# Kernel tuning notes

Hardware: AMD Instinct MI355X
Metric: run time of the kernel (lower is better)

Reference implementation:

```python
import jax, jax.numpy as jnp
import numpy as np

B, T, U = 64, 400, 64
V, E, H = 80, 128, 400
M, K = 10, 20  # attention mixtures, output mixtures


def _lstm_cell(x, h, c, W_ih, W_hh, b_ih, b_hh):
    g = x @ W_ih.T + b_ih + h @ W_hh.T + b_hh
    i, f, gg, o = jnp.split(g, 4, axis=-1)
    c_new = jax.nn.sigmoid(f) * c + jax.nn.sigmoid(i) * jnp.tanh(gg)
    h_new = jax.nn.sigmoid(o) * jnp.tanh(c_new)
    return h_new, c_new


def setup_inputs() -> dict:
    key = jax.random.key(0)
    ks = jax.random.split(key, 16)
    s = 0.05
    inp = {
        'strokes': jax.random.normal(ks[0], (B, T, 3), jnp.float32),
        'chars': jax.random.randint(ks[1], (B, U), 0, V, jnp.int32),
        'chars_mask': jnp.ones((B, U), jnp.float32),
        'emb': jax.random.normal(ks[2], (V, E)) * s,
        # layer_0: input 3+E
        'W_ih0': jax.random.normal(ks[3], (4 * H, 3 + E)) * s,
        'W_hh0': jax.random.normal(ks[4], (4 * H, H)) * s,
        'b_ih0': jnp.zeros((4 * H,)), 'b_hh0': jnp.zeros((4 * H,)),
        # layer_n[0], layer_n[1]: input 3+E+H
        'W_ih1': jax.random.normal(ks[5], (4 * H, 3 + E + H)) * s,
        'W_hh1': jax.random.normal(ks[6], (4 * H, H)) * s,
        'b_ih1': jnp.zeros((4 * H,)), 'b_hh1': jnp.zeros((4 * H,)),
        'W_ih2': jax.random.normal(ks[7], (4 * H, 3 + E + H)) * s,
        'W_hh2': jax.random.normal(ks[8], (4 * H, H)) * s,
        'b_ih2': jnp.zeros((4 * H,)), 'b_hh2': jnp.zeros((4 * H,)),
        # Gaussian attention linear: H -> 3M
        'Wa': jax.random.normal(ks[9], (3 * M, H)) * s,
        'ba': jnp.zeros((3 * M,)),
        # output linear: 3H -> 6K+1
        'Wo': jax.random.normal(ks[10], (6 * K + 1, 3 * H)) * s,
        'bo': jnp.zeros((6 * K + 1,)),
        # learned initial states
        'h0': jnp.zeros((3, H)), 'c0': jnp.zeros((3, H)),
        'w0': jnp.zeros((E,)), 'k0': jnp.zeros((M,)),
    }
    return inp


def _forward(strokes, chars, chars_mask, emb, W_ih0, W_hh0, b_ih0, b_hh0,
             W_ih1, W_hh1, b_ih1, b_hh1, W_ih2, W_hh2, b_ih2, b_hh2,
             Wa, ba, Wo, bo, h0, c0, w0, k0):
    ctx = emb[chars] * chars_mask[:, :, None]            # (B,U,E)
    u = jnp.arange(U, dtype=jnp.float32)                 # (U,)
    bsz = strokes.shape[0]

    def attn(h_t, k_tm1):
        p = jnp.exp(h_t @ Wa.T + ba)                     # (B,3M)
        alpha, beta, kappa = jnp.split(p, 3, axis=-1)    # (B,M) each
        kappa = kappa + k_tm1
        # phi: (B,U)
        phi = jnp.sum(alpha[:, None, :] * jnp.exp(-beta[:, None, :]
                      * (kappa[:, None, :] - u[None, :, None]) ** 2), axis=-1)
        w = jnp.sum(phi[:, :, None] * ctx, axis=1)       # (B,E)
        return w, kappa

    bc = lambda v: jnp.broadcast_to(v, (bsz,) + v.shape)
    carry0 = (bc(h0[0]), bc(h0[1]), bc(h0[2]),
              bc(c0[0]), bc(c0[1]), bc(c0[2]), bc(w0), bc(k0))

    def step(carry, x_t):
        h0_, h1_, h2_, c0_, c1_, c2_, w_, k_ = carry
        # layer_0
        hA, cA = _lstm_cell(jnp.concatenate([x_t, w_], 1), h0_, c0_,
                            W_ih0, W_hh0, b_ih0, b_hh0)
        w_n, k_n = attn(hA, k_)
        # faithful replication of source's buggy layer_n loop (j starts at 0):
        # j=0: input uses h_tm1[-1] (slot2), prev state = slot1, writes slot0
        n0h, n0c = _lstm_cell(jnp.concatenate([x_t, w_n, h2_], 1), h1_, c1_,
                              W_ih1, W_hh1, b_ih1, b_hh1)
        # j=1: input uses h_tm1[0] (just written), prev state = slot2, writes slot1
        n1h, n1c = _lstm_cell(jnp.concatenate([x_t, w_n, n0h], 1), h2_, c2_,
                              W_ih2, W_hh2, b_ih2, b_hh2)
        # slot2 never updated; output uses [slot0, slot1, slot2]
        out = jnp.concatenate([n0h, n1h, h2_], 1) @ Wo.T + bo
        return (n0h, n1h, h2_, n0c, n1c, c2_, w_n, k_n), out

    _, outs = jax.lax.scan(step, carry0, jnp.swapaxes(strokes, 0, 1))
    out = jnp.swapaxes(outs, 0, 1)                       # (B,T,6K+1)

    mu, log_sigma, pi, rho_raw, eos = jnp.split(
        out, [2 * K, 4 * K, 5 * K, 6 * K], axis=-1)
    sigma = jnp.exp(log_sigma).reshape(out.shape[0], out.shape[1], K, 2)
    mu = mu.reshape(out.shape[0], out.shape[1], K, 2)
    rho = jnp.tanh(rho_raw)                              # (B,T,K)
    log_pi = jax.nn.log_softmax(pi, axis=-1)

    x = strokes[:, :, None, :2]                          # (B,T,1,2)
    t = (x - mu) / sigma                                 # (B,T,K,2)
    Z = jnp.sum(t ** 2, -1) - 2.0 * rho * t[..., 0] * t[..., 1]
    num = -Z / (2.0 * (1.0 - rho ** 2))
    denom = (np.log(2 * np.pi) + jnp.sum(jnp.log(sigma), -1)
             + 0.5 * jnp.log(1.0 - rho ** 2))
    log_N = num - denom
    stroke_loss = jnp.mean(-jax.nn.logsumexp(log_pi + log_N, axis=-1))

    y = strokes[:, :, 2:3]
    z = eos
    eos_loss = jnp.mean(jnp.maximum(z, 0.0) - z * y
                        + jnp.log1p(jnp.exp(-jnp.abs(z))))
    return jnp.stack([stroke_loss, eos_loss])


def reference(strokes, chars, chars_mask, emb, W_ih0, W_hh0, b_ih0, b_hh0,
              W_ih1, W_hh1, b_ih1, b_hh1, W_ih2, W_hh2, b_ih2, b_hh2,
              Wa, ba, Wo, bo, h0, c0, w0, k0):
    return _forward(strokes, chars, chars_mask, emb, W_ih0, W_hh0, b_ih0,
                    b_hh0, W_ih1, W_hh1, b_ih1, b_hh1, W_ih2, W_hh2, b_ih2,
                    b_hh2, Wa, ba, Wo, bo, h0, c0, w0, k0)
```

## Files before the change

kernel.cpp:

```cpp
#include <hip/hip_runtime.h>
#include <hip/hip_bf16.h>


#define B_ 64
#define T_ 400
#define U_ 64
#define E_ 128
#define H_ 400
#define M_ 10
#define NO_ 121

#define NBLK 100
#define NTHR 512

constexpr size_t OF_WS2  = 128;
constexpr size_t OF_KS   = OF_WS2 + 64*128;
constexpr size_t OF_N0H  = OF_KS + 640;
constexpr size_t OF_N0C  = OF_N0H + 25600;
constexpr size_t OF_N1H  = OF_N0C + 25600;
constexpr size_t OF_N1C  = OF_N1H + 25600;
constexpr size_t OF_HA   = OF_N1C + 25600;
constexpr size_t OF_B0   = OF_HA + 25600;
constexpr size_t OF_B1   = OF_B0 + 1600;
constexpr size_t OF_B2   = OF_B1 + 1600;
constexpr size_t OF_OB   = OF_B2 + 1600;
constexpr size_t OF_XT   = OF_OB + 128;
constexpr size_t OF_CTX  = OF_XT + (size_t)T_*3*64;
constexpr size_t OF_A0   = OF_CTX + (size_t)64*64*128;
constexpr size_t OF_A1   = OF_A0 + (size_t)T_*64*400/2;
constexpr size_t WS_FLOATS = OF_A1 + (size_t)T_*64*400/2;

__device__ __forceinline__ float sigf(float x) { return 1.f/(1.f + expf(-x)); }

__device__ __forceinline__ float ld_dev(const float* p) {
  unsigned v = __hip_atomic_load((const unsigned*)p, __ATOMIC_RELAXED, __HIP_MEMORY_SCOPE_AGENT);
  return __uint_as_float(v);
}
__device__ __forceinline__ float2 ld_dev2(const float* p) {
  unsigned long long v = __hip_atomic_load((const unsigned long long*)p, __ATOMIC_RELAXED, __HIP_MEMORY_SCOPE_AGENT);
  union { unsigned long long u; float2 f; } c; c.u = v; return c.f;
}
__device__ __forceinline__ void st_dev(float* p, float v) {
  __hip_atomic_store((unsigned*)p, __float_as_uint(v), __ATOMIC_RELAXED, __HIP_MEMORY_SCOPE_AGENT);
}

__device__ __forceinline__ void gbar(unsigned* cnt, unsigned* gen, unsigned tgt) {
  __syncthreads();
  if (threadIdx.x == 0) {
    unsigned prev = __hip_atomic_fetch_add(cnt, 1u, __ATOMIC_RELAXED, __HIP_MEMORY_SCOPE_AGENT);
    if (prev == tgt*(unsigned)NBLK - 1u) {
      __hip_atomic_store(gen, tgt, __ATOMIC_RELAXED, __HIP_MEMORY_SCOPE_AGENT);
    } else {
      while (__hip_atomic_load(gen, __ATOMIC_RELAXED, __HIP_MEMORY_SCOPE_AGENT) < tgt)
        __builtin_amdgcn_s_sleep(4);
    }
  }
  __syncthreads();
}

__global__ void k_pre(
  const float* __restrict__ strokes, const int* __restrict__ chars, const float* __restrict__ cmask,
  const float* __restrict__ emb,
  const float* __restrict__ Wih1, const float* __restrict__ Whh2, const float* __restrict__ Wo,
  const float* __restrict__ bih0, const float* __restrict__ bhh0,
  const float* __restrict__ bih1, const float* __restrict__ bhh1,
  const float* __restrict__ bih2, const float* __restrict__ bhh2,
  const float* __restrict__ bo,
  const float* __restrict__ h0, const float* __restrict__ c0,
  const float* __restrict__ w0, const float* __restrict__ k0,
  float* __restrict__ ws)
{
  const int gid = blockIdx.x*blockDim.x + threadIdx.x;
  const int gsz = gridDim.x*blockDim.x;
  float* ctxp = ws + OF_CTX;
  for (int i = gid; i < 64*64*128; i += gsz) {
    int b = i >> 13, rem = i & 8191, u = rem >> 7, e = rem & 127;
    ctxp[i] = emb[chars[b*64+u]*128+e] * cmask[b*64+u];
  }
  float* xT = ws + OF_XT;
  for (int i = gid; i < T_*3*64; i += gsz) {
    int t = i/192, r = i - t*192, j = r >> 6, b = r & 63;
    xT[i] = strokes[(b*T_+t)*3+j];
  }
  const float* h2c = h0 + 800;
  float* b0 = ws + OF_B0; float* b1 = ws + OF_B1; float* b2 = ws + OF_B2;
  for (int r = gid; r < 1600; r += gsz) {
    b0[r] = bih0[r] + bhh0[r];
    float s1 = bih1[r] + bhh1[r];
    const float* w1 = Wih1 + (size_t)r*531 + 131;
    for (int j = 0; j < 400; ++j) s1 += w1[j]*h2c[j];
    b1[r] = s1;
    float s2 = bih2[r] + bhh2[r];
    const float* w2 = Whh2 + (size_t)r*400;
    for (int j = 0; j < 400; ++j) s2 += w2[j]*h2c[j];
    b2[r] = s2;
  }
  float* ob = ws + OF_OB;
  for (int r = gid; r < 121; r += gsz) {
    float s = bo[r];
    const float* wr = Wo + (size_t)r*1200 + 800;
    for (int j = 0; j < 400; ++j) s += wr[j]*h2c[j];
    ob[r] = s;
  }
  float* wS = ws + OF_WS2;
  for (int i = gid; i < 8192; i += gsz) wS[i] = w0[i & 127];
  float* kS = ws + OF_KS;
  for (int i = gid; i < 640; i += gsz) kS[i] = k0[i % 10];
  float* n1hp = ws + OF_N1H; float* n1cp = ws + OF_N1C;
  for (int i = gid; i < 25600; i += gsz) {
    n1hp[i] = h0[400 + (i % 400)];
    n1cp[i] = c0[400 + (i >> 6)];
  }
}

__global__ __launch_bounds__(512) void k_init(
  const float* __restrict__ Wih0, const float* __restrict__ Whh0,
  const float* __restrict__ h0, const float* __restrict__ c0, const float* __restrict__ w0,
  float* __restrict__ ws)
{
  const int lane = threadIdx.x & 63;
  const int wv = threadIdx.x >> 6;
  const int n = blockIdx.x*8 + wv;
  if (n >= 400) return;
  const float* bias0 = ws + OF_B0;
  const float* xT = ws + OF_XT;
  float* hA = ws + OF_HA;
  float g[4];
  #pragma unroll
  for (int q = 0; q < 4; ++q) {
    int r = q*400 + n;
    const float* wi = Wih0 + (size_t)r*131;
    const float* wh = Whh0 + (size_t)r*400;
    float a = bias0[r];
    a += xT[0*64+lane]*wi[0] + xT[1*64+lane]*wi[1] + xT[2*64+lane]*wi[2];
    for (int e = 0; e < 128; ++e) a += w0[e]*wi[3+e];
    for (int j = 0; j < 400; ++j) a += h0[j]*wh[j];
    g[q] = a;
  }
  float cn = sigf(g[1])*c0[n] + sigf(g[0])*tanhf(g[2]);
  hA[lane*400 + n] = sigf(g[3])*tanhf(cn);
}

__device__ __forceinline__ void gemv8(
    int xt_idx, int lane, int kq, int rh, int ns, int ch,
    const float* __restrict__ bias,
    const float* __restrict__ Wxw, int sxw,
    const float* __restrict__ Whh, int shh, int hoff,
    const float* __restrict__ xT,
    const float* hLs, const float* wLs, float* pLs)
{
  const int hrows = 2*ch;
  float acc[8]; const float* wrow[8];
  #pragma unroll
  for (int s = 0; s < 8; ++s) {
    if (s < hrows) {
      int rr = rh*hrows + s;
      int q = rr / ch, nl = rr - q*ch;
      int r = __builtin_amdgcn_readfirstlane(q*H_ + ns + nl);
      if (kq == 0) { wrow[s] = Wxw + (size_t)r*sxw;        acc[s] = bias[r]; }
      else         { wrow[s] = Whh + (size_t)r*shh + hoff; acc[s] = 0.f; }
    }
  }
  if (kq == 0) {
    float x0 = xT[(xt_idx*3+0)*64+lane];
    float x1 = xT[(xt_idx*3+1)*64+lane];
    float x2 = xT[(xt_idx*3+2)*64+lane];
    #pragma unroll
    for (int s = 0; s < 8; ++s) if (s < hrows)
      acc[s] += x0*wrow[s][0] + x1*wrow[s][1] + x2*wrow[s][2];
    #pragma unroll 2
    for (int ec = 0; ec < 32; ++ec) {
      float4 w4 = *(const float4*)&wLs[lane*132 + ec*4];
      #pragma unroll
      for (int s = 0; s < 8; ++s) if (s < hrows) {
        const float* wp = wrow[s] + 3 + ec*4;
        acc[s] += w4.x*wp[0] + w4.y*wp[1] + w4.z*wp[2] + w4.w*wp[3];
      }
    }
  } else {
    int jb = (kq==1) ? 0 : (kq==2 ? 33 : 66);
    int je = (kq==1) ? 33 : (kq==2 ? 66 : 100);
    #pragma unroll 2
    for (int jc = jb; jc < je; ++jc) {
      float4 hv = *(const float4*)&hLs[lane*404 + jc*4];
      #pragma unroll
      for (int s = 0; s < 8; ++s) if (s < hrows) {
        const float* wp = wrow[s] + jc*4;
        acc[s] += hv.x*wp[0] + hv.y*wp[1] + hv.z*wp[2] + hv.w*wp[3];
      }
    }
  }
  #pragma unroll
  for (int s = 0; s < 8; ++s) if (s < hrows)
    pLs[((rh*4+kq)*8 + s)*64 + lane] = acc[s];
}

__global__ __launch_bounds__(NTHR) void k_scan(
  const float* __restrict__ Wih0, const float* __restrict__ Whh0,
  const float* __restrict__ Wih1, const float* __restrict__ Whh1,
  const float* __restrict__ Wih2,
  const float* __restrict__ Wa, const float* __restrict__ ba,
  const float* __restrict__ c0, float* __restrict__ ws)
{
  __shared__ __align__(16) float hLs[64*404];
  __shared__ __align__(16) float wLs[64*132];
  __shared__ float pLs[8*8*64];
  __shared__ float hab[400];
  __shared__ float aScr[32];
  __shared__ float phL[64];

  const int tid = threadIdx.x;
  const int lane = tid & 63;
  const int wv = __builtin_amdgcn_readfirstlane(tid >> 6);
  const int kq = wv & 3, rh = wv >> 2;
  const int bid = blockIdx.x;
  const int ns = bid*4;

  unsigned* ctrl = (unsigned*)ws;
  unsigned* cnt = &ctrl[0];
  unsigned* gen = &ctrl[32];
  float* wS  = ws + OF_WS2;
  float* kS  = ws + OF_KS;
  float* n0h = ws + OF_N0H; float* n0c = ws + OF_N0C;
  float* n1h = ws + OF_N1H; float* n1c = ws + OF_N1C;
  float* hA  = ws + OF_HA;
  const float* bias0 = ws + OF_B0;
  const float* bias1 = ws + OF_B1;
  const float* bias2 = ws + OF_B2;
  const float* xT  = ws + OF_XT;
  const float* ctx = ws + OF_CTX;
  __hip_bfloat16* a0 = (__hip_bfloat16*)(ws + OF_A0);
  __hip_bfloat16* a1 = (__hip_bfloat16*)(ws + OF_A1);

  unsigned bgen = 0;

  for (int t = 0; t < T_; ++t) {
    if (bid < 64) {
      if (wv == 0) {
        const int b = bid;
        for (int i = lane; i < 200; i += 64) {
          float2 v = ld_dev2(&hA[b*400 + i*2]);
          *(float2*)&hab[i*2] = v;
        }
        asm volatile("s_waitcnt vmcnt(0) lgkmcnt(0)" ::: "memory");
        float s = 0.f;
        if (lane < 30) {
          const float* wr = Wa + lane*400;
          #pragma unroll 4
          for (int j = 0; j < 400; ++j) s += hab[j]*wr[j];
          s += ba[lane];
        }
        float p = expf(s);
        float val = p;
        if (lane >= 20 && lane < 30) {
          float kap = p + kS[b*10 + (lane-20)];
          kS[b*10 + (lane-20)] = kap;
          val = kap;
        }
        if (lane < 30) aScr[lane] = val;
        asm volatile("s_waitcnt lgkmcnt(0)" ::: "memory");
        float uu = (float)lane, ph = 0.f;
        #pragma unroll
        for (int m = 0; m < 10; ++m) {
          float d = aScr[20+m] - uu;
          ph += aScr[m] * expf(-aScr[10+m]*d*d);
        }
        phL[lane] = ph;
        asm volatile("s_waitcnt lgkmcnt(0)" ::: "memory");
        float a0w = 0.f, a1w = 0.f;
        const float* cb = ctx + (size_t)b*8192;
        for (int u2 = 0; u2 < 64; ++u2) {
          float phv = phL[u2];
          a0w += phv * cb[u2*128 + lane];
          a1w += phv * cb[u2*128 + 64 + lane];
        }
        st_dev(&wS[b*128 + lane], a0w);
        st_dev(&wS[b*128 + 64 + lane], a1w);
      } else {
        for (int i = tid - 64; i < 12800; i += (NTHR-64)) {
          int b2 = i/200, jc = i - b2*200;
          float2 v = ld_dev2(&n1h[b2*400 + jc*2]);
          *(float2*)&hLs[b2*404 + jc*2] = v;
        }
      }
    } else {
      for (int i = tid; i < 12800; i += NTHR) {
        int b2 = i/200, jc = i - b2*200;
        float2 v = ld_dev2(&n1h[b2*400 + jc*2]);
        *(float2*)&hLs[b2*404 + jc*2] = v;
      }
    }
    gbar(cnt, gen, ++bgen);

    for (int i = tid; i < 4096; i += NTHR) {
      int b2 = i >> 6, ec = i & 63;
      float2 v = ld_dev2(&wS[b2*128 + ec*2]);
      *(float2*)&wLs[b2*132 + ec*2] = v;
    }
    __syncthreads();
    gemv8(t, lane, kq, rh, ns, 4, bias1, Wih1, 531, Whh1, 400, 0, xT, hLs, wLs, pLs);
    __syncthreads();
    for (int i = tid; i < 256; i += NTHR) {
      int nl = i >> 6, b = i & 63, n = ns+nl;
      float g[4];
      #pragma unroll
      for (int q = 0; q < 4; ++q) {
        int rr = q*4+nl; int r2 = (rr >= 8); int s = rr - r2*8;
        float v = 0.f;
        #pragma unroll
        for (int k2 = 0; k2 < 4; ++k2) v += pLs[((r2*4+k2)*8+s)*64+b];
        g[q] = v;
      }
      float cp = n1c[n*64+b];
      float cn = sigf(g[1])*cp + sigf(g[0])*tanhf(g[2]);
      float hn = sigf(g[3])*tanhf(cn);
      n0c[n*64+b] = cn;
      st_dev(&n0h[b*400+n], hn);
      a0[((size_t)t*64+b)*400+n] = __float2bfloat16(hn);
    }
    gbar(cnt, gen, ++bgen);

    for (int i = tid; i < 12800; i += NTHR) {
      int b2 = i/200, jc = i - b2*200;
      float2 v = ld_dev2(&n0h[b2*400 + jc*2]);
      *(float2*)&hLs[b2*404 + jc*2] = v;
    }
    __syncthreads();
    gemv8(t, lane, kq, rh, ns, 4, bias2, Wih2, 531, Wih2, 531, 131, xT, hLs, wLs, pLs);
    __syncthreads();
    for (int i = tid; i < 256; i += NTHR) {
      int nl = i >> 6, b = i & 63, n = ns+nl;
      float g[4];
      #pragma unroll
      for (int q = 0; q < 4; ++q) {
        int rr = q*4+nl; int r2 = (rr >= 8); int s = rr - r2*8;
        float v = 0.f;
        #pragma unroll
        for (int k2 = 0; k2 < 4; ++k2) v += pLs[((r2*4+k2)*8+s)*64+b];
        g[q] = v;
      }
      float cn = sigf(g[1])*c0[800+n] + sigf(g[0])*tanhf(g[2]);
      float hn = sigf(g[3])*tanhf(cn);
      n1c[n*64+b] = cn;
      st_dev(&n1h[b*400+n], hn);
      a1[((size_t)t*64+b)*400+n] = __float2bfloat16(hn);
    }
    __syncthreads();
    if (t < T_-1) {
      gemv8(t+1, lane, kq, rh, ns, 4, bias0, Wih0, 131, Whh0, 400, 0, xT, hLs, wLs, pLs);
      __syncthreads();
      for (int i = tid; i < 256; i += NTHR) {
        int nl = i >> 6, b = i & 63, n = ns+nl;
        float g[4];
        #pragma unroll
        for (int q = 0; q < 4; ++q) {
          int rr = q*4+nl; int r2 = (rr >= 8); int s = rr - r2*8;
          float v = 0.f;
          #pragma unroll
          for (int k2 = 0; k2 < 4; ++k2) v += pLs[((r2*4+k2)*8+s)*64+b];
          g[q] = v;
        }
        float cp = n0c[n*64+b];
        float cn = sigf(g[1])*cp + sigf(g[0])*tanhf(g[2]);
        st_dev(&hA[b*400+n], sigf(g[3])*tanhf(cn));
      }
    }
    gbar(cnt, gen, ++bgen);
  }
}

__global__ __launch_bounds__(NTHR) void k_outloss(
  const float* __restrict__ Wo, const float* __restrict__ strokes, float* __restrict__ ws)
{
  __shared__ __align__(16) float hL4[64*404];
  __shared__ float oL[121*65];
  const int t = blockIdx.x;
  const int tid = threadIdx.x;
  const int lane = tid & 63;
  const int wv = __builtin_amdgcn_readfirstlane(tid >> 6);
  const float* ob = ws + OF_OB;
  const __hip_bfloat16* a0 = (const __hip_bfloat16*)(ws + OF_A0);
  const __hip_bfloat16* a1 = (const __hip_bfloat16*)(ws + OF_A1);

  float acc[16];
  #pragma unroll
  for (int s = 0; s < 16; ++s) { int r = wv + 8*s; acc[s] = (r < 121) ? ob[r] : 0.f; }

  const unsigned* src0 = (const unsigned*)(a0 + (size_t)t*25600);
  for (int i = tid; i < 12800; i += NTHR) {
    unsigned v = src0[i];
    int b = i/200, jc = i - b*200;
    hL4[b*404+jc*2+0] = __uint_as_float(v << 16);
    hL4[b*404+jc*2+1] = __uint_as_float(v & 0xffff0000u);
  }
  __syncthreads();
  for (int jc = 0; jc < 100; ++jc) {
    float4 hv = *(const float4*)&hL4[lane*404+jc*4];
    #pragma unroll
    for (int s = 0; s < 16; ++s) {
      int r = wv + 8*s;
      if (r < 121) {
        const float* wp = Wo + (size_t)r*1200 + jc*4;
        acc[s] += hv.x*wp[0] + hv.y*wp[1] + hv.z*wp[2] + hv.w*wp[3];
      }
    }
  }
  __syncthreads();
  const unsigned* src1 = (const unsigned*)(a1 + (size_t)t*25600);
  for (int i = tid; i < 12800; i += NTHR) {
    unsigned v = src1[i];
    int b = i/200, jc = i - b*200;
    hL4[b*404+jc*2+0] = __uint_as_float(v << 16);
    hL4[b*404+jc*2+1] = __uint_as_float(v & 0xffff0000u);
  }
  __syncthreads();
  for (int jc = 0; jc < 100; ++jc) {
    float4 hv = *(const float4*)&hL4[lane*404+jc*4];
    #pragma unroll
    for (int s = 0; s < 16; ++s) {
      int r = wv + 8*s;
      if (r < 121) {
        const float* wp = Wo + (size_t)r*1200 + 400 + jc*4;
        acc[s] += hv.x*wp[0] + hv.y*wp[1] + hv.z*wp[2] + hv.w*wp[3];
      }
    }
  }
  #pragma unroll
  for (int s = 0; s < 16; ++s) { int r = wv + 8*s; if (r < 121) oL[r*65+lane] = acc[s]; }
  __syncthreads();

  if (wv == 0) {
    const int b = lane;
    float x0 = strokes[(b*T_+t)*3+0];
    float x1 = strokes[(b*T_+t)*3+1];
    float y  = strokes[(b*T_+t)*3+2];
    float mp = -1e30f;
    #pragma unroll
    for (int k = 0; k < 20; ++k) mp = fmaxf(mp, oL[(80+k)*65+b]);
    float sp = 0.f;
    #pragma unroll
    for (int k = 0; k < 20; ++k) sp += expf(oL[(80+k)*65+b] - mp);
    float lsep = mp + logf(sp);
    float sk[20]; float ms = -1e30f;
    #pragma unroll
    for (int k = 0; k < 20; ++k) {
      float mu0 = oL[(2*k)*65+b],    mu1 = oL[(2*k+1)*65+b];
      float l0  = oL[(40+2*k)*65+b], l1  = oL[(41+2*k)*65+b];
      float rho = tanhf(oL[(100+k)*65+b]);
      float t0 = (x0-mu0)*expf(-l0);
      float t1 = (x1-mu1)*expf(-l1);
      float on = 1.f - rho*rho;
      float Z = t0*t0 + t1*t1 - 2.f*rho*t0*t1;
      float logN = -Z/(2.f*on) - (1.8378770664093453f + l0 + l1 + 0.5f*logf(on));
      float sv = (oL[(80+k)*65+b] - lsep) + logN;
      sk[k] = sv; ms = fmaxf(ms, sv);
    }
    float ss = 0.f;
    #pragma unroll
    for (int k = 0; k < 20; ++k) ss += expf(sk[k]-ms);
    float stroke = -(ms + logf(ss));
    float z = oL[120*65+b];
    float eos = fmaxf(z,0.f) - z*y + log1pf(expf(-fabsf(z)));
    #pragma unroll
    for (int off = 32; off > 0; off >>= 1) {
      stroke += __shfl_down(stroke, off, 64);
      eos    += __shfl_down(eos, off, 64);
    }
    if (lane == 0) { atomicAdd(ws+64, stroke); atomicAdd(ws+65, eos); }
  }
}

__global__ void k_fin(const float* __restrict__ ws, float* __restrict__ out) {
  if (threadIdx.x == 0) {
    out[0] = ws[64] * (1.f/25600.f);
    out[1] = ws[65] * (1.f/25600.f);
  }
}

extern "C" void kernel_launch(void* const* d_in, const int* in_sizes, int n_in,
                              void* d_out, int out_size, void* d_ws, size_t ws_size,
                              hipStream_t stream) {
  const float* strokes = (const float*)d_in[0];
  const int*   chars   = (const int*)d_in[1];
  const float* cmask   = (const float*)d_in[2];
  const float* emb     = (const float*)d_in[3];
  const float* Wih0    = (const float*)d_in[4];
  const float* Whh0    = (const float*)d_in[5];
  const float* bih0    = (const float*)d_in[6];
  const float* bhh0    = (const float*)d_in[7];
  const float* Wih1    = (const float*)d_in[8];
  const float* Whh1    = (const float*)d_in[9];
  const float* bih1    = (const float*)d_in[10];
  const float* bhh1    = (const float*)d_in[11];
  const float* Wih2    = (const float*)d_in[12];
  const float* Whh2    = (const float*)d_in[13];
  const float* bih2    = (const float*)d_in[14];
  const float* bhh2    = (const float*)d_in[15];
  const float* Wa      = (const float*)d_in[16];
  const float* ba      = (const float*)d_in[17];
  const float* Wo      = (const float*)d_in[18];
  const float* bo      = (const float*)d_in[19];
  const float* h0      = (const float*)d_in[20];
  const float* c0      = (const float*)d_in[21];
  const float* w0      = (const float*)d_in[22];
  const float* k0      = (const float*)d_in[23];
  float* ws = (float*)d_ws;
  float* out = (float*)d_out;
  if (ws_size < WS_FLOATS*sizeof(float)) return;

  hipMemsetAsync(d_ws, 0, 512, stream);
  k_pre<<<256, 256, 0, stream>>>(strokes, chars, cmask, emb, Wih1, Whh2, Wo,
                                 bih0, bhh0, bih1, bhh1, bih2, bhh2, bo,
                                 h0, c0, w0, k0, ws);
  k_init<<<50, 512, 0, stream>>>(Wih0, Whh0, h0, c0, w0, ws);
  k_scan<<<NBLK, NTHR, 0, stream>>>(Wih0, Whh0, Wih1, Whh1, Wih2, Wa, ba, c0, ws);
  k_outloss<<<T_, NTHR, 0, stream>>>(Wo, strokes, ws);
  k_fin<<<1, 64, 0, stream>>>(ws, out);
}
```

Baseline: 41.35 ms.

## Replace atomic grid barrier with flag barrier and overlap attention with recurrent GEMV

Swaps the counter-based grid barrier for per-block flags spaced across cache lines, with block 0 gathering them and broadcasting a release flag. The separate barrier after attention becomes a point-to-point flag wait, so the Whh1 product runs while attention finishes. The input-side GEMVs for layers 0 and 2 are hoisted to share the staged attention window, and h staging uses wide dwordx4 cache-bypassing loads and stores. Each step now has two global barriers instead of three, at the cost of more register pressure and a more delicate memory-ordering scheme.

```diff
diff --git a/kernel.cpp b/kernel.cpp
--- a/kernel.cpp
+++ b/kernel.cpp
@@ -2,19 +2,18 @@
 #include <hip/hip_bf16.h>
 
 
+typedef float f4 __attribute__((ext_vector_type(4)));
+
 #define B_ 64
 #define T_ 400
-#define U_ 64
-#define E_ 128
 #define H_ 400
-#define M_ 10
-#define NO_ 121
-
 #define NBLK 100
 #define NTHR 512
-
-constexpr size_t OF_WS2  = 128;
-constexpr size_t OF_KS   = OF_WS2 + 64*128;
+#define FLW 32
+
+constexpr size_t OF_LOSS = 5312;
+constexpr size_t OF_WS2  = 8192;
+constexpr size_t OF_KS   = OF_WS2 + 8192;
 constexpr size_t OF_N0H  = OF_KS + 640;
 constexpr size_t OF_N0C  = OF_N0H + 25600;
 constexpr size_t OF_N1H  = OF_N0C + 25600;
@@ -32,30 +31,76 @@
 
 __device__ __forceinline__ float sigf(float x) { return 1.f/(1.f + expf(-x)); }
 
-__device__ __forceinline__ float ld_dev(const float* p) {
-  unsigned v = __hip_atomic_load((const unsigned*)p, __ATOMIC_RELAXED, __HIP_MEMORY_SCOPE_AGENT);
-  return __uint_as_float(v);
-}
-__device__ __forceinline__ float2 ld_dev2(const float* p) {
-  unsigned long long v = __hip_atomic_load((const unsigned long long*)p, __ATOMIC_RELAXED, __HIP_MEMORY_SCOPE_AGENT);
-  union { unsigned long long u; float2 f; } c; c.u = v; return c.f;
-}
-__device__ __forceinline__ void st_dev(float* p, float v) {
-  __hip_atomic_store((unsigned*)p, __float_as_uint(v), __ATOMIC_RELAXED, __HIP_MEMORY_SCOPE_AGENT);
-}
-
-__device__ __forceinline__ void gbar(unsigned* cnt, unsigned* gen, unsigned tgt) {
+__device__ __forceinline__ void ldg4(f4& d, const float* p) {
+  asm volatile("global_load_dwordx4 %0, %1, off sc0 sc1" : "=v"(d) : "v"(p));
+}
+__device__ __forceinline__ void stg4(float* p, f4 v) {
+  asm volatile("global_store_dwordx4 %0, %1, off sc0 sc1" :: "v"(p), "v"(v) : "memory");
+}
+__device__ __forceinline__ void stg1(float* p, float v) {
+  asm volatile("global_store_dword %0, %1, off sc0 sc1" :: "v"(p), "v"(v) : "memory");
+}
+__device__ __forceinline__ void waitv0() {
+  asm volatile("s_waitcnt vmcnt(0)" ::: "memory");
+  __builtin_amdgcn_sched_barrier(0);
+}
+__device__ __forceinline__ unsigned ldf(const unsigned* p) {
+  return __hip_atomic_load(p, __ATOMIC_RELAXED, __HIP_MEMORY_SCOPE_AGENT);
+}
+__device__ __forceinline__ void stf(unsigned* p, unsigned v) {
+  __hip_atomic_store(p, v, __ATOMIC_RELAXED, __HIP_MEMORY_SCOPE_AGENT);
+}
+
+__device__ __forceinline__ void stage_h(const float* __restrict__ g, float* lds, int tid) {
+  f4 v[13];
+  const float* pa[13];
+  #pragma unroll
+  for (int k = 0; k < 13; ++k) {
+    int u = tid + k*512;
+    int uu = (u < 6400) ? u : 6399;
+    int b = uu/100, jc = uu - b*100;
+    pa[k] = g + b*400 + jc*4;
+  }
+  #pragma unroll
+  for (int k = 0; k < 13; ++k) ldg4(v[k], pa[k]);
+  waitv0();
+  #pragma unroll
+  for (int k = 0; k < 13; ++k) {
+    int u = tid + k*512;
+    if (u < 6400) { int b = u/100, jc = u - b*100; *(f4*)&lds[b*404 + jc*4] = v[k]; }
+  }
+}
+
+__device__ __forceinline__ void gbar(unsigned* ctrl, int bid, unsigned tgt,
+                                     int tid, int lane, int wv) {
   __syncthreads();
-  if (threadIdx.x == 0) {
-    unsigned prev = __hip_atomic_fetch_add(cnt, 1u, __ATOMIC_RELAXED, __HIP_MEMORY_SCOPE_AGENT);
-    if (prev == tgt*(unsigned)NBLK - 1u) {
-      __hip_atomic_store(gen, tgt, __ATOMIC_RELAXED, __HIP_MEMORY_SCOPE_AGENT);
-    } else {
-      while (__hip_atomic_load(gen, __ATOMIC_RELAXED, __HIP_MEMORY_SCOPE_AGENT) < tgt)
-        __builtin_amdgcn_s_sleep(4);
-    }
+  if (tid == 0) {
+    asm volatile("s_waitcnt vmcnt(0)" ::: "memory");
+    stf(&ctrl[FLW*(1+bid)], tgt);
+  }
+  if (bid == 0) {
+    if (wv == 0) {
+      bool on = (lane < 50);
+      const unsigned* f0 = &ctrl[FLW*(1+2*lane)];
+      const unsigned* f1 = &ctrl[FLW*(2+2*lane)];
+      for (;;) {
+        unsigned a = on ? ldf(f0) : tgt;
+        unsigned b = on ? ldf(f1) : tgt;
+        if (__all((int)(a >= tgt && b >= tgt))) break;
+        __builtin_amdgcn_s_sleep(1);
+      }
+      if (lane == 0) stf(&ctrl[0], tgt);
+    }
+  } else if (tid == 0) {
+    while (ldf(&ctrl[0]) < tgt) __builtin_amdgcn_s_sleep(1);
   }
   __syncthreads();
+}
+
+__device__ __forceinline__ unsigned bfu(float x) {
+  union { __hip_bfloat16 h; unsigned short u; } c;
+  c.h = __float2bfloat16(x);
+  return (unsigned)c.u;
 }
 
 __global__ void k_pre(
@@ -102,8 +147,6 @@
     for (int j = 0; j < 400; ++j) s += wr[j]*h2c[j];
     ob[r] = s;
   }
-  float* wS = ws + OF_WS2;
-  for (int i = gid; i < 8192; i += gsz) wS[i] = w0[i & 127];
   float* kS = ws + OF_KS;
   for (int i = gid; i < 640; i += gsz) kS[i] = k0[i % 10];
   float* n1hp = ws + OF_N1H; float* n1cp = ws + OF_N1C;
@@ -141,61 +184,7 @@
   hA[lane*400 + n] = sigf(g[3])*tanhf(cn);
 }
 
-__device__ __forceinline__ void gemv8(
-    int xt_idx, int lane, int kq, int rh, int ns, int ch,
-    const float* __restrict__ bias,
-    const float* __restrict__ Wxw, int sxw,
-    const float* __restrict__ Whh, int shh, int hoff,
-    const float* __restrict__ xT,
-    const float* hLs, const float* wLs, float* pLs)
-{
-  const int hrows = 2*ch;
-  float acc[8]; const float* wrow[8];
-  #pragma unroll
-  for (int s = 0; s < 8; ++s) {
-    if (s < hrows) {
-      int rr = rh*hrows + s;
-      int q = rr / ch, nl = rr - q*ch;
-      int r = __builtin_amdgcn_readfirstlane(q*H_ + ns + nl);
-      if (kq == 0) { wrow[s] = Wxw + (size_t)r*sxw;        acc[s] = bias[r]; }
-      else         { wrow[s] = Whh + (size_t)r*shh + hoff; acc[s] = 0.f; }
-    }
-  }
-  if (kq == 0) {
-    float x0 = xT[(xt_idx*3+0)*64+lane];
-    float x1 = xT[(xt_idx*3+1)*64+lane];
-    float x2 = xT[(xt_idx*3+2)*64+lane];
-    #pragma unroll
-    for (int s = 0; s < 8; ++s) if (s < hrows)
-      acc[s] += x0*wrow[s][0] + x1*wrow[s][1] + x2*wrow[s][2];
-    #pragma unroll 2
-    for (int ec = 0; ec < 32; ++ec) {
-      float4 w4 = *(const float4*)&wLs[lane*132 + ec*4];
-      #pragma unroll
-      for (int s = 0; s < 8; ++s) if (s < hrows) {
-        const float* wp = wrow[s] + 3 + ec*4;
-        acc[s] += w4.x*wp[0] + w4.y*wp[1] + w4.z*wp[2] + w4.w*wp[3];
-      }
-    }
-  } else {
-    int jb = (kq==1) ? 0 : (kq==2 ? 33 : 66);
-    int je = (kq==1) ? 33 : (kq==2 ? 66 : 100);
-    #pragma unroll 2
-    for (int jc = jb; jc < je; ++jc) {
-      float4 hv = *(const float4*)&hLs[lane*404 + jc*4];
-      #pragma unroll
-      for (int s = 0; s < 8; ++s) if (s < hrows) {
-        const float* wp = wrow[s] + jc*4;
-        acc[s] += hv.x*wp[0] + hv.y*wp[1] + hv.z*wp[2] + hv.w*wp[3];
-      }
-    }
-  }
-  #pragma unroll
-  for (int s = 0; s < 8; ++s) if (s < hrows)
-    pLs[((rh*4+kq)*8 + s)*64 + lane] = acc[s];
-}
-
-__global__ __launch_bounds__(NTHR) void k_scan(
+__global__ __launch_bounds__(NTHR, 2) void k_scan(
   const float* __restrict__ Wih0, const float* __restrict__ Whh0,
   const float* __restrict__ Wih1, const float* __restrict__ Whh1,
   const float* __restrict__ Wih2,
@@ -205,20 +194,20 @@
   __shared__ __align__(16) float hLs[64*404];
   __shared__ __align__(16) float wLs[64*132];
   __shared__ float pLs[8*8*64];
-  __shared__ float hab[400];
+  __shared__ __align__(16) float hab[400];
   __shared__ float aScr[32];
   __shared__ float phL[64];
 
-  const int tid = threadIdx.x;
+  const int tid  = threadIdx.x;
   const int lane = tid & 63;
-  const int wv = __builtin_amdgcn_readfirstlane(tid >> 6);
-  const int kq = wv & 3, rh = wv >> 2;
-  const int bid = blockIdx.x;
-  const int ns = bid*4;
+  const int wv   = __builtin_amdgcn_readfirstlane(tid >> 6);
+  const int kq   = wv & 3, rh = wv >> 2;
+  const int rh2  = wv & 1, kc = wv >> 1;
+  const int bid  = blockIdx.x;
+  const int ns   = bid*4;
+  const bool isAttn = (bid < 64);
 
   unsigned* ctrl = (unsigned*)ws;
-  unsigned* cnt = &ctrl[0];
-  unsigned* gen = &ctrl[32];
   float* wS  = ws + OF_WS2;
   float* kS  = ws + OF_KS;
   float* n0h = ws + OF_N0H; float* n0c = ws + OF_N0C;
@@ -227,145 +216,294 @@
   const float* bias0 = ws + OF_B0;
   const float* bias1 = ws + OF_B1;
   const float* bias2 = ws + OF_B2;
+  const float* c2c = c0 + 800;
   const float* xT  = ws + OF_XT;
   const float* ctx = ws + OF_CTX;
-  __hip_bfloat16* a0 = (__hip_bfloat16*)(ws + OF_A0);
-  __hip_bfloat16* a1 = (__hip_bfloat16*)(ws + OF_A1);
-
-  unsigned bgen = 0;
+  unsigned short* a0 = (unsigned short*)(ws + OF_A0);
+  unsigned short* a1 = (unsigned short*)(ws + OF_A1);
+
+  float acc1[8], acc2[8], acc0[8];
+  unsigned tgt = 0;
 
   for (int t = 0; t < T_; ++t) {
-    if (bid < 64) {
-      if (wv == 0) {
-        const int b = bid;
-        for (int i = lane; i < 200; i += 64) {
-          float2 v = ld_dev2(&hA[b*400 + i*2]);
-          *(float2*)&hab[i*2] = v;
-        }
-        asm volatile("s_waitcnt vmcnt(0) lgkmcnt(0)" ::: "memory");
-        float s = 0.f;
-        if (lane < 30) {
-          const float* wr = Wa + lane*400;
-          #pragma unroll 4
-          for (int j = 0; j < 400; ++j) s += hab[j]*wr[j];
-          s += ba[lane];
-        }
-        float p = expf(s);
-        float val = p;
-        if (lane >= 20 && lane < 30) {
-          float kap = p + kS[b*10 + (lane-20)];
-          kS[b*10 + (lane-20)] = kap;
-          val = kap;
-        }
-        if (lane < 30) aScr[lane] = val;
-        asm volatile("s_waitcnt lgkmcnt(0)" ::: "memory");
-        float uu = (float)lane, ph = 0.f;
-        #pragma unroll
-        for (int m = 0; m < 10; ++m) {
-          float d = aScr[20+m] - uu;
-          ph += aScr[m] * expf(-aScr[10+m]*d*d);
-        }
-        phL[lane] = ph;
-        asm volatile("s_waitcnt lgkmcnt(0)" ::: "memory");
-        float a0w = 0.f, a1w = 0.f;
-        const float* cb = ctx + (size_t)b*8192;
-        for (int u2 = 0; u2 < 64; ++u2) {
-          float phv = phL[u2];
-          a0w += phv * cb[u2*128 + lane];
-          a1w += phv * cb[u2*128 + 64 + lane];
-        }
-        st_dev(&wS[b*128 + lane], a0w);
-        st_dev(&wS[b*128 + 64 + lane], a1w);
-      } else {
-        for (int i = tid - 64; i < 12800; i += (NTHR-64)) {
-          int b2 = i/200, jc = i - b2*200;
-          float2 v = ld_dev2(&n1h[b2*400 + jc*2]);
-          *(float2*)&hLs[b2*404 + jc*2] = v;
-        }
-      }
-    } else {
-      for (int i = tid; i < 12800; i += NTHR) {
-        int b2 = i/200, jc = i - b2*200;
-        float2 v = ld_dev2(&n1h[b2*400 + jc*2]);
-        *(float2*)&hLs[b2*404 + jc*2] = v;
-      }
-    }
-    gbar(cnt, gen, ++bgen);
-
-    for (int i = tid; i < 4096; i += NTHR) {
-      int b2 = i >> 6, ec = i & 63;
-      float2 v = ld_dev2(&wS[b2*128 + ec*2]);
-      *(float2*)&wLs[b2*132 + ec*2] = v;
-    }
-    __syncthreads();
-    gemv8(t, lane, kq, rh, ns, 4, bias1, Wih1, 531, Whh1, 400, 0, xT, hLs, wLs, pLs);
-    __syncthreads();
-    for (int i = tid; i < 256; i += NTHR) {
-      int nl = i >> 6, b = i & 63, n = ns+nl;
-      float g[4];
-      #pragma unroll
-      for (int q = 0; q < 4; ++q) {
-        int rr = q*4+nl; int r2 = (rr >= 8); int s = rr - r2*8;
-        float v = 0.f;
-        #pragma unroll
-        for (int k2 = 0; k2 < 4; ++k2) v += pLs[((r2*4+k2)*8+s)*64+b];
-        g[q] = v;
-      }
-      float cp = n1c[n*64+b];
-      float cn = sigf(g[1])*cp + sigf(g[0])*tanhf(g[2]);
-      float hn = sigf(g[3])*tanhf(cn);
-      n0c[n*64+b] = cn;
-      st_dev(&n0h[b*400+n], hn);
-      a0[((size_t)t*64+b)*400+n] = __float2bfloat16(hn);
-    }
-    gbar(cnt, gen, ++bgen);
-
-    for (int i = tid; i < 12800; i += NTHR) {
-      int b2 = i/200, jc = i - b2*200;
-      float2 v = ld_dev2(&n0h[b2*400 + jc*2]);
-      *(float2*)&hLs[b2*404 + jc*2] = v;
-    }
-    __syncthreads();
-    gemv8(t, lane, kq, rh, ns, 4, bias2, Wih2, 531, Wih2, 531, 131, xT, hLs, wLs, pLs);
-    __syncthreads();
-    for (int i = tid; i < 256; i += NTHR) {
-      int nl = i >> 6, b = i & 63, n = ns+nl;
-      float g[4];
-      #pragma unroll
-      for (int q = 0; q < 4; ++q) {
-        int rr = q*4+nl; int r2 = (rr >= 8); int s = rr - r2*8;
-        float v = 0.f;
-        #pragma unroll
-        for (int k2 = 0; k2 < 4; ++k2) v += pLs[((r2*4+k2)*8+s)*64+b];
-        g[q] = v;
-      }
-      float cn = sigf(g[1])*c0[800+n] + sigf(g[0])*tanhf(g[2]);
-      float hn = sigf(g[3])*tanhf(cn);
-      n1c[n*64+b] = cn;
-      st_dev(&n1h[b*400+n], hn);
-      a1[((size_t)t*64+b)*400+n] = __float2bfloat16(hn);
-    }
-    __syncthreads();
-    if (t < T_-1) {
-      gemv8(t+1, lane, kq, rh, ns, 4, bias0, Wih0, 131, Whh0, 400, 0, xT, hLs, wLs, pLs);
-      __syncthreads();
-      for (int i = tid; i < 256; i += NTHR) {
-        int nl = i >> 6, b = i & 63, n = ns+nl;
+    stage_h(n1h, hLs, tid);
+    __syncthreads();
+
+    if (isAttn && wv == 0) {
+      const int b = bid;
+      f4 v0, v1;
+      const float* p0 = &hA[b*400 + lane*4];
+      bool on1 = (lane < 36);
+      const float* p1 = on1 ? &hA[b*400 + 256 + lane*4] : p0;
+      ldg4(v0, p0); ldg4(v1, p1);
+      waitv0();
+      *(f4*)&hab[lane*4] = v0;
+      if (on1) *(f4*)&hab[256 + lane*4] = v1;
+      asm volatile("s_waitcnt lgkmcnt(0)" ::: "memory");
+      float s = 0.f;
+      if (lane < 30) {
+        const float* wr = Wa + lane*400;
+        #pragma unroll 4
+        for (int j = 0; j < 400; ++j) s += hab[j]*wr[j];
+        s += ba[lane];
+      }
+      float p = expf(s);
+      float val = p;
+      if (lane >= 20 && lane < 30) {
+        float kap = p + kS[b*10 + (lane-20)];
+        kS[b*10 + (lane-20)] = kap;
+        val = kap;
+      }
+      if (lane < 30) aScr[lane] = val;
+      asm volatile("s_waitcnt lgkmcnt(0)" ::: "memory");
+      float uu = (float)lane, ph = 0.f;
+      #pragma unroll
+      for (int m = 0; m < 10; ++m) {
+        float d = aScr[20+m] - uu;
+        ph += aScr[m] * expf(-aScr[10+m]*d*d);
+      }
+      phL[lane] = ph;
+      asm volatile("s_waitcnt lgkmcnt(0)" ::: "memory");
+      float a0w = 0.f, a1w = 0.f;
+      const float* cb = ctx + (size_t)b*8192;
+      for (int u2 = 0; u2 < 64; ++u2) {
+        float phv = phL[u2];
+        a0w += phv * cb[u2*128 + lane];
+        a1w += phv * cb[u2*128 + 64 + lane];
+      }
+      stg1(&wS[b*128 + lane], a0w);
+      stg1(&wS[b*128 + 64 + lane], a1w);
+      asm volatile("s_waitcnt vmcnt(0)" ::: "memory");
+      if (lane == 0) stf(&ctrl[FLW*(101+b)], (unsigned)(t+1));
+    }
+
+    #pragma unroll
+    for (int s = 0; s < 8; ++s) acc1[s] = 0.f;
+    if (kq != 0) {
+      const float* wr[8];
+      #pragma unroll
+      for (int s = 0; s < 8; ++s) {
+        int rr = rh*8+s;
+        int r = __builtin_amdgcn_readfirstlane((rr>>2)*H_ + ns + (rr&3));
+        wr[s] = Whh1 + (size_t)r*400;
+      }
+      int jb = (kq==1)?0:(kq==2?33:66);
+      int je = (kq==1)?33:(kq==2?66:100);
+      for (int jc = jb; jc < je; ++jc) {
+        f4 hv = *(const f4*)&hLs[lane*404 + jc*4];
+        #pragma unroll
+        for (int s = 0; s < 8; ++s) {
+          const float* wp = wr[s] + jc*4;
+          acc1[s] += hv.x*wp[0] + hv.y*wp[1] + hv.z*wp[2] + hv.w*wp[3];
+        }
+      }
+    }
+    __syncthreads();
+
+    if (wv == 0) {
+      const unsigned* af = &ctrl[FLW*(101+lane)];
+      while (!__all((int)(ldf(af) >= (unsigned)(t+1))))
+        __builtin_amdgcn_s_sleep(1);
+    }
+    __syncthreads();
+
+    {
+      f4 v0,v1,v2,v3;
+      int u0=tid, u1=tid+512, u2=tid+1024, u3=tid+1536;
+      ldg4(v0, &wS[(u0>>5)*128+(u0&31)*4]);
+      ldg4(v1, &wS[(u1>>5)*128+(u1&31)*4]);
+      ldg4(v2, &wS[(u2>>5)*128+(u2&31)*4]);
+      ldg4(v3, &wS[(u3>>5)*128+(u3&31)*4]);
+      waitv0();
+      *(f4*)&wLs[(u0>>5)*132+(u0&31)*4] = v0;
+      *(f4*)&wLs[(u1>>5)*132+(u1&31)*4] = v1;
+      *(f4*)&wLs[(u2>>5)*132+(u2&31)*4] = v2;
+      *(f4*)&wLs[(u3>>5)*132+(u3&31)*4] = v3;
+    }
+    __syncthreads();
+
+    {
+      const float* wr1[8];
+      #pragma unroll
+      for (int s = 0; s < 8; ++s) {
+        int rr = rh*8+s;
+        int r = __builtin_amdgcn_readfirstlane((rr>>2)*H_ + ns + (rr&3));
+        wr1[s] = Wih1 + (size_t)r*531;
+        if (kq == 0) acc1[s] += bias1[r];
+      }
+      if (kq == 0) {
+        float x0 = xT[(t*3+0)*64+lane], x1 = xT[(t*3+1)*64+lane], x2 = xT[(t*3+2)*64+lane];
+        #pragma unroll
+        for (int s = 0; s < 8; ++s)
+          acc1[s] += x0*wr1[s][0] + x1*wr1[s][1] + x2*wr1[s][2];
+      }
+      for (int f = kq*8; f < kq*8+8; ++f) {
+        f4 w4 = *(const f4*)&wLs[lane*132 + f*4];
+        #pragma unroll
+        for (int s = 0; s < 8; ++s) {
+          const float* wp = wr1[s] + 3 + f*4;
+          acc1[s] += w4.x*wp[0] + w4.y*wp[1] + w4.z*wp[2] + w4.w*wp[3];
+        }
+      }
+      const float* wr2[8]; const float* wr0[8];
+      #pragma unroll
+      for (int s = 0; s < 8; ++s) {
+        int rr = rh2*8+s;
+        int r = __builtin_amdgcn_readfirstlane((rr>>2)*H_ + ns + (rr&3));
+        wr2[s] = Wih2 + (size_t)r*531;
+        wr0[s] = Wih0 + (size_t)r*131;
+        if (kc == 0) { acc2[s] = bias2[r]; acc0[s] = bias0[r]; }
+        else         { acc2[s] = 0.f;      acc0[s] = 0.f; }
+      }
+      if (kc == 0) {
+        int tn = (t < T_-1) ? t+1 : t;
+        float x0 = xT[(t*3+0)*64+lane], x1 = xT[(t*3+1)*64+lane], x2 = xT[(t*3+2)*64+lane];
+        float y0 = xT[(tn*3+0)*64+lane], y1 = xT[(tn*3+1)*64+lane], y2 = xT[(tn*3+2)*64+lane];
+        #pragma unroll
+        for (int s = 0; s < 8; ++s) {
+          acc2[s] += x0*wr2[s][0] + x1*wr2[s][1] + x2*wr2[s][2];
+          acc0[s] += y0*wr0[s][0] + y1*wr0[s][1] + y2*wr0[s][2];
+        }
+      }
+      for (int f = kc*8; f < kc*8+8; ++f) {
+        f4 w4 = *(const f4*)&wLs[lane*132 + f*4];
+        #pragma unroll
+        for (int s = 0; s < 8; ++s) {
+          const float* wp2 = wr2[s] + 3 + f*4;
+          acc2[s] += w4.x*wp2[0] + w4.y*wp2[1] + w4.z*wp2[2] + w4.w*wp2[3];
+          const float* wp0 = wr0[s] + 3 + f*4;
+          acc0[s] += w4.x*wp0[0] + w4.y*wp0[1] + w4.z*wp0[2] + w4.w*wp0[3];
+        }
+      }
+      #pragma unroll
+      for (int s = 0; s < 8; ++s)
+        pLs[((rh*4+kq)*8+s)*64+lane] = acc1[s];
+    }
+    __syncthreads();
+
+    if (tid < 64) {
+      const int b = tid;
+      float hv[4];
+      #pragma unroll
+      for (int nl = 0; nl < 4; ++nl) {
         float g[4];
         #pragma unroll
         for (int q = 0; q < 4; ++q) {
-          int rr = q*4+nl; int r2 = (rr >= 8); int s = rr - r2*8;
+          int rr = q*4+nl, rhh = rr>>3, s = rr&7;
           float v = 0.f;
           #pragma unroll
-          for (int k2 = 0; k2 < 4; ++k2) v += pLs[((r2*4+k2)*8+s)*64+b];
+          for (int k2 = 0; k2 < 4; ++k2) v += pLs[((rhh*4+k2)*8+s)*64+b];
           g[q] = v;
         }
-        float cp = n0c[n*64+b];
+        float cp = n1c[(ns+nl)*64+b];
         float cn = sigf(g[1])*cp + sigf(g[0])*tanhf(g[2]);
-        st_dev(&hA[b*400+n], sigf(g[3])*tanhf(cn));
-      }
-    }
-    gbar(cnt, gen, ++bgen);
+        n0c[(ns+nl)*64+b] = cn;
+        hv[nl] = sigf(g[3])*tanhf(cn);
+      }
+      f4 o = {hv[0],hv[1],hv[2],hv[3]};
+      stg4(&n0h[b*400+ns], o);
+      uint2 pk;
+      pk.x = (bfu(hv[1])<<16) | bfu(hv[0]);
+      pk.y = (bfu(hv[3])<<16) | bfu(hv[2]);
+      *(uint2*)(a0 + ((size_t)t*64+b)*400 + ns) = pk;
+    }
+    gbar(ctrl, bid, ++tgt, tid, lane, wv);
+
+    stage_h(n0h, hLs, tid);
+    __syncthreads();
+
+    {
+      const float* wr[8];
+      #pragma unroll
+      for (int s = 0; s < 8; ++s) {
+        int rr = rh2*8+s;
+        int r = __builtin_amdgcn_readfirstlane((rr>>2)*H_ + ns + (rr&3));
+        wr[s] = Wih2 + (size_t)r*531 + 131;
+      }
+      for (int jc = kc*25; jc < kc*25+25; ++jc) {
+        f4 hv = *(const f4*)&hLs[lane*404 + jc*4];
+        #pragma unroll
+        for (int s = 0; s < 8; ++s) {
+          const float* wp = wr[s] + jc*4;
+          acc2[s] += hv.x*wp[0] + hv.y*wp[1] + hv.z*wp[2] + hv.w*wp[3];
+        }
+      }
+      #pragma unroll
+      for (int s = 0; s < 8; ++s)
+        pLs[((rh2*4+kc)*8+s)*64+lane] = acc2[s];
+    }
+    __syncthreads();
+
+    if (tid < 64) {
+      const int b = tid;
+      float hv[4];
+      #pragma unroll
+      for (int nl = 0; nl < 4; ++nl) {
+        float g[4];
+        #pragma unroll
+        for (int q = 0; q < 4; ++q) {
+          int rr = q*4+nl, rhh = rr>>3, s = rr&7;
+          float v = 0.f;
+          #pragma unroll
+          for (int k2 = 0; k2 < 4; ++k2) v += pLs[((rhh*4+k2)*8+s)*64+b];
+          g[q] = v;
+        }
+        float cn = sigf(g[1])*c2c[ns+nl] + sigf(g[0])*tanhf(g[2]);
+        n1c[(ns+nl)*64+b] = cn;
+        hv[nl] = sigf(g[3])*tanhf(cn);
+      }
+      f4 o = {hv[0],hv[1],hv[2],hv[3]};
+      stg4(&n1h[b*400+ns], o);
+      uint2 pk;
+      pk.x = (bfu(hv[1])<<16) | bfu(hv[0]);
+      pk.y = (bfu(hv[3])<<16) | bfu(hv[2]);
+      *(uint2*)(a1 + ((size_t)t*64+b)*400 + ns) = pk;
+    }
+    __syncthreads();
+
+    if (t < T_-1) {
+      const float* wr[8];
+      #pragma unroll
+      for (int s = 0; s < 8; ++s) {
+        int rr = rh2*8+s;
+        int r = __builtin_amdgcn_readfirstlane((rr>>2)*H_ + ns + (rr&3));
+        wr[s] = Whh0 + (size_t)r*400;
+      }
+      for (int jc = kc*25; jc < kc*25+25; ++jc) {
+        f4 hv = *(const f4*)&hLs[lane*404 + jc*4];
+        #pragma unroll
+        for (int s = 0; s < 8; ++s) {
+          const float* wp = wr[s] + jc*4;
+          acc0[s] += hv.x*wp[0] + hv.y*wp[1] + hv.z*wp[2] + hv.w*wp[3];
+        }
+      }
+      #pragma unroll
+      for (int s = 0; s < 8; ++s)
+        pLs[((rh2*4+kc)*8+s)*64+lane] = acc0[s];
+      __syncthreads();
+      if (tid < 64) {
+        const int b = tid;
+        float hv[4];
+        #pragma unroll
+        for (int nl = 0; nl < 4; ++nl) {
+          float g[4];
+          #pragma unroll
+          for (int q = 0; q < 4; ++q) {
+            int rr = q*4+nl, rhh = rr>>3, s = rr&7;
+            float v = 0.f;
+            #pragma unroll
+            for (int k2 = 0; k2 < 4; ++k2) v += pLs[((rhh*4+k2)*8+s)*64+b];
+            g[q] = v;
+          }
+          float cp = n0c[(ns+nl)*64+b];
+          float cn = sigf(g[1])*cp + sigf(g[0])*tanhf(g[2]);
+          hv[nl] = sigf(g[3])*tanhf(cn);
+        }
+        f4 o = {hv[0],hv[1],hv[2],hv[3]};
+        stg4(&hA[b*400+ns], o);
+      }
+    }
+    gbar(ctrl, bid, ++tgt, tid, lane, wv);
   }
 }
 
@@ -379,14 +517,13 @@
   const int lane = tid & 63;
   const int wv = __builtin_amdgcn_readfirstlane(tid >> 6);
   const float* ob = ws + OF_OB;
-  const __hip_bfloat16* a0 = (const __hip_bfloat16*)(ws + OF_A0);
-  const __hip_bfloat16* a1 = (const __hip_bfloat16*)(ws + OF_A1);
+  const unsigned* src0 = (const unsigned*)(ws + OF_A0) + (size_t)t*12800;
+  const unsigned* src1 = (const unsigned*)(ws + OF_A1) + (size_t)t*12800;
 
   float acc[16];
   #pragma unroll
   for (int s = 0; s < 16; ++s) { int r = wv + 8*s; acc[s] = (r < 121) ? ob[r] : 0.f; }
 
-  const unsigned* src0 = (const unsigned*)(a0 + (size_t)t*25600);
   for (int i = tid; i < 12800; i += NTHR) {
     unsigned v = src0[i];
     int b = i/200, jc = i - b*200;
@@ -395,7 +532,7 @@
   }
   __syncthreads();
   for (int jc = 0; jc < 100; ++jc) {
-    float4 hv = *(const float4*)&hL4[lane*404+jc*4];
+    f4 hv = *(const f4*)&hL4[lane*404+jc*4];
     #pragma unroll
     for (int s = 0; s < 16; ++s) {
       int r = wv + 8*s;
@@ -406,7 +543,6 @@
     }
   }
   __syncthreads();
-  const unsigned* src1 = (const unsigned*)(a1 + (size_t)t*25600);
   for (int i = tid; i < 12800; i += NTHR) {
     unsigned v = src1[i];
     int b = i/200, jc = i - b*200;
@@ -415,7 +551,7 @@
   }
   __syncthreads();
   for (int jc = 0; jc < 100; ++jc) {
-    float4 hv = *(const float4*)&hL4[lane*404+jc*4];
+    f4 hv = *(const f4*)&hL4[lane*404+jc*4];
     #pragma unroll
     for (int s = 0; s < 16; ++s) {
       int r = wv + 8*s;
@@ -466,14 +602,14 @@
       stroke += __shfl_down(stroke, off, 64);
       eos    += __shfl_down(eos, off, 64);
     }
-    if (lane == 0) { atomicAdd(ws+64, stroke); atomicAdd(ws+65, eos); }
+    if (lane == 0) { atomicAdd(ws+OF_LOSS, stroke); atomicAdd(ws+OF_LOSS+1, eos); }
   }
 }
 
 __global__ void k_fin(const float* __restrict__ ws, float* __restrict__ out) {
   if (threadIdx.x == 0) {
-    out[0] = ws[64] * (1.f/25600.f);
-    out[1] = ws[65] * (1.f/25600.f);
+    out[0] = ws[OF_LOSS]   * (1.f/25600.f);
+    out[1] = ws[OF_LOSS+1] * (1.f/25600.f);
   }
 }
 
@@ -508,7 +644,7 @@
   float* out = (float*)d_out;
   if (ws_size < WS_FLOATS*sizeof(float)) return;
 
-  hipMemsetAsync(d_ws, 0, 512, stream);
+  hipMemsetAsync(d_ws, 0, 32768, stream);
   k_pre<<<256, 256, 0, stream>>>(strokes, chars, cmask, emb, Wih1, Whh2, Wo,
                                  bih0, bhh0, bih1, bhh1, bih2, bhh2, bo,
                                  h0, c0, w0, k0, ws);
```

Result: faster. 37.39 ms (-9.6%).
